# Optimization experiments

Measured on AMD Instinct MI355X. Metric: run time of the kernel, lower is better.

## Reference

```python
import jax, jax.numpy as jnp
import numpy as np

B, S, H = 4, 4096, 2048


def setup_inputs() -> dict:
    key = jax.random.key(0)
    ks = jax.random.split(key, 20)
    def lin(k, fin, fout):
        # torch nn.Linear default init: U(-1/sqrt(fin), 1/sqrt(fin))
        kw, kb = jax.random.split(k)
        bound = 1.0 / np.sqrt(fin)
        W = jax.random.uniform(kw, (fin, fout), jnp.float32, -bound, bound)
        b = jax.random.uniform(kb, (fout,), jnp.float32, -bound, bound)
        return W, b
    hidden_states = jax.random.normal(ks[0], (B, S, H), jnp.float32)
    access_frequency = jax.random.uniform(ks[1], (B, S), jnp.float32)
    importance_score = jax.random.uniform(ks[2], (B, S), jnp.float32)
    sel_W1, sel_b1 = lin(ks[3], H, H // 4)
    sel_W2, sel_b2 = lin(ks[4], H // 4, 3)
    c1_W, c1_b = lin(ks[5], H, H // 2)
    f1_W, f1_b = lin(ks[6], H // 2, H // 2)
    d1_W, d1_b = lin(ks[7], H // 2, H)
    c2_W, c2_b = lin(ks[8], H, H // 4)
    f2_W, f2_b = lin(ks[9], H // 4, H // 4)
    d2_W, d2_b = lin(ks[10], H // 4, H)
    return dict(hidden_states=hidden_states, access_frequency=access_frequency,
                importance_score=importance_score, sel_W1=sel_W1, sel_b1=sel_b1,
                sel_W2=sel_W2, sel_b2=sel_b2, c1_W=c1_W, c1_b=c1_b, f1_W=f1_W,
                f1_b=f1_b, d1_W=d1_W, d1_b=d1_b, c2_W=c2_W, c2_b=c2_b,
                f2_W=f2_W, f2_b=f2_b, d2_W=d2_W, d2_b=d2_b)


def reference(hidden_states, access_frequency, importance_score,
              sel_W1, sel_b1, sel_W2, sel_b2,
              c1_W, c1_b, f1_W, f1_b, d1_W, d1_b,
              c2_W, c2_b, f2_W, f2_b, d2_W, d2_b):
    x = hidden_states  # [B,S,H]
    Hh = x.shape[-1] // 2
    # strategy selector on frequency/importance-modulated features
    combined = jnp.concatenate(
        [x[..., :Hh] * access_frequency[..., None],
         x[..., Hh:] * importance_score[..., None]], axis=-1)  # [B,S,H]
    hmid = jax.nn.relu(jnp.einsum('bsh,hk->bsk', combined, sel_W1) + sel_b1)
    weights = jax.nn.softmax(jnp.einsum('bsk,kl->bsl', hmid, sel_W2) + sel_b2)
    sel = jnp.argmax(weights, axis=-1)  # [B,S] in {0,1,2}
    # expert paths (computed densely, selected per token)
    out1 = (jax.numpy.einsum('bsh,hc->bsc', x, c1_W) + c1_b)
    out1 = jnp.einsum('bsc,cd->bsd', out1, f1_W) + f1_b
    out1 = jnp.einsum('bsc,ch->bsh', out1, d1_W) + d1_b
    out2 = (jnp.einsum('bsh,hc->bsc', x, c2_W) + c2_b)
    out2 = jnp.einsum('bsc,cd->bsd', out2, f2_W) + f2_b
    out2 = jnp.einsum('bsc,ch->bsh', out2, d2_W) + d2_b
    s = sel[..., None]
    out = jnp.where(s == 0, x, jnp.where(s == 1, out1, out2))
    return out
```

## Files before the change

### kernel.cpp

```cpp
#include <hip/hip_runtime.h>


#define RECHECK_TAU 0.008

typedef __bf16 bf16x8 __attribute__((ext_vector_type(8)));
typedef float  f32x4  __attribute__((ext_vector_type(4)));
typedef unsigned short us;

__device__ __forceinline__ float bf2f(us u) {
  union { unsigned u; float f; } v; v.u = ((unsigned)u) << 16;
  return v.f;
}
__device__ __forceinline__ us f2bf(float f) {
  union { float f; unsigned u; } v; v.f = f;
  unsigned r = v.u + 0x7fffu + ((v.u >> 16) & 1u);
  return (us)(r >> 16);
}
__device__ __forceinline__ float scrub(float v) {
  return (v == v && fabsf(v) < 1e30f) ? v : 0.f;
}
__device__ __forceinline__ void gld_lds16(const void* g, void* l) {
  __builtin_amdgcn_global_load_lds(
      (const __attribute__((address_space(1))) void*)g,
      (__attribute__((address_space(3))) void*)l, 16, 0, 0);
}

__global__ __launch_bounds__(256) void xprep(
    const float* __restrict__ X, const float* __restrict__ FR,
    const float* __restrict__ IM, us* __restrict__ Xb, us* __restrict__ Xm)
{
  const int t = blockIdx.x;
  const int j = threadIdx.x;
  const float fr = FR[t], im = IM[t];
  const float md = (j < 128) ? fr : im;
  const float4* src = (const float4*)(X + (size_t)t * 2048);
  float4 a0 = src[2 * j], a1 = src[2 * j + 1];
  float av[8] = {a0.x, a0.y, a0.z, a0.w, a1.x, a1.y, a1.z, a1.w};
  union { uint4 v; us u[8]; } b, m;
#pragma unroll
  for (int k = 0; k < 8; ++k) {
    b.u[k] = f2bf(av[k]);
    m.u[k] = f2bf(av[k] * md);
  }
  ((uint4*)(Xb + (size_t)t * 2048))[j] = b.v;
  ((uint4*)(Xm + (size_t)t * 2048))[j] = m.v;
}

template<int MODE, int AIDX>
__global__ __launch_bounds__(256) void gemm_bt(
    const us* __restrict__ Ap, const us* __restrict__ BT,
    const float* __restrict__ bias, void* __restrict__ outp,
    const int* __restrict__ aidx, const int* __restrict__ oidx,
    const int* __restrict__ cntp, int N, int K)
{
  const int cnt = cntp ? cntp[0] : (int)(gridDim.x << 7);
  const int Mp  = (cnt + 127) & ~127;
  const int bm0 = blockIdx.x * 128;
  if (bm0 >= Mp) return;
  const int bn0 = blockIdx.y * 128;

  __shared__ __align__(16) us As[128 * 64];
  __shared__ __align__(16) us Bs[128 * 64];
  const int tid  = threadIdx.x;
  const int lane = tid & 63;
  const int w    = tid >> 6;
  const int wr   = w >> 1, wc = w & 1;

  const us* gb[4];
  const us* ga[4];
  us* la[4]; us* lb[4];
#pragma unroll
  for (int i = 0; i < 4; ++i) {
    const int s = i * 256 + tid, m = s >> 3, cp = s & 7, c = cp ^ (m & 7);
    gb[i] = BT + (size_t)(bn0 + m) * K + c * 8;
    lb[i] = &Bs[s * 8];
    la[i] = &As[s * 8];
    const int arow = AIDX ? aidx[bm0 + m] : (bm0 + m);
    ga[i] = Ap + (size_t)arow * K + c * 8;
  }

  f32x4 acc[4][4] = {};

  for (int k0 = 0; k0 < K; k0 += 64) {
#pragma unroll
    for (int i = 0; i < 4; ++i) { gld_lds16(gb[i], lb[i]); gb[i] += 64; }
#pragma unroll
    for (int i = 0; i < 4; ++i) { gld_lds16(ga[i], la[i]); ga[i] += 64; }
    __syncthreads();
#pragma unroll
    for (int kk = 0; kk < 2; ++kk) {
      const int cc = kk * 4 + (lane >> 4);
      bf16x8 af[4], bfr[4];
#pragma unroll
      for (int t = 0; t < 4; ++t) {
        const int m = wr * 64 + t * 16 + (lane & 15);
        const int n = wc * 64 + t * 16 + (lane & 15);
        af[t]  = *(const bf16x8*)&As[(m * 8 + (cc ^ (m & 7))) * 8];
        bfr[t] = *(const bf16x8*)&Bs[(n * 8 + (cc ^ (n & 7))) * 8];
      }
#pragma unroll
      for (int mt = 0; mt < 4; ++mt)
#pragma unroll
        for (int nt = 0; nt < 4; ++nt)
          acc[mt][nt] = __builtin_amdgcn_mfma_f32_16x16x32_bf16(
              af[mt], bfr[nt], acc[mt][nt], 0, 0, 0);
    }
    __syncthreads();
  }

  const int colb = bn0 + wc * 64 + (lane & 15);
  const int rowb = bm0 + wr * 64 + ((lane >> 4) << 2);
  float bv[4];
#pragma unroll
  for (int nt = 0; nt < 4; ++nt) bv[nt] = bias[colb + nt * 16];
#pragma unroll
  for (int mt = 0; mt < 4; ++mt) {
#pragma unroll
    for (int r = 0; r < 4; ++r) {
      const int row = rowb + mt * 16 + r;
      if (MODE == 3) {
        if (row >= cnt) continue;
        const size_t orow = (size_t)oidx[row];
#pragma unroll
        for (int nt = 0; nt < 4; ++nt)
          ((float*)outp)[orow * N + colb + nt * 16] =
              scrub(acc[mt][nt][r] + bv[nt]);
      } else if (MODE == 4) {
#pragma unroll
        for (int nt = 0; nt < 4; ++nt)
          ((float*)outp)[(size_t)row * N + colb + nt * 16] =
              fmaxf(scrub(acc[mt][nt][r] + bv[nt]), 0.f);
      } else {
#pragma unroll
        for (int nt = 0; nt < 4; ++nt)
          ((us*)outp)[(size_t)row * N + colb + nt * 16] =
              f2bf(scrub(acc[mt][nt][r] + bv[nt]));
      }
    }
  }
}

__global__ __launch_bounds__(256) void sel_precise(
    const float* __restrict__ X, const float* __restrict__ FR,
    const float* __restrict__ IM,
    const us* __restrict__ BTH, const us* __restrict__ BTL,
    const float* __restrict__ bias, float* __restrict__ hmid_r,
    const int* __restrict__ ridx, const int* __restrict__ cntp)
{
  constexpr int K = 2048, N = 512;
  const int cnt = cntp[0];
  const int Mp  = (cnt + 127) & ~127;
  const int bm0 = blockIdx.x * 128;
  if (bm0 >= Mp) return;
  const int bn0 = blockIdx.y * 128;

  __shared__ __align__(16) us AsH[128 * 64];
  __shared__ __align__(16) us AsL[128 * 64];
  __shared__ __align__(16) us BsH[128 * 64];
  __shared__ __align__(16) us BsL[128 * 64];
  const int tid  = threadIdx.x;
  const int lane = tid & 63;
  const int w    = tid >> 6;
  const int wr   = w >> 1, wc = w & 1;

  const us* gbh[4]; const us* gbl[4];
  const float* gx[4];
  us* lbh[4]; us* lbl[4];
  int sOfs[4], cth[4];
  float fr[4], im[4];
#pragma unroll
  for (int i = 0; i < 4; ++i) {
    const int s = i * 256 + tid, m = s >> 3, cp = s & 7, c = cp ^ (m & 7);
    gbh[i] = BTH + (size_t)(bn0 + m) * K + c * 8;
    gbl[i] = BTL + (size_t)(bn0 + m) * K + c * 8;
    lbh[i] = &BsH[s * 8];
    lbl[i] = &BsL[s * 8];
    const int arow = ridx[bm0 + m];
    gx[i]  = X + (size_t)arow * K + c * 8;
    sOfs[i] = s * 8;
    cth[i]  = c * 8;
    fr[i] = FR[arow];
    im[i] = IM[arow];
  }

  f32x4 acc[4][4] = {};

  for (int k0 = 0; k0 < K; k0 += 64) {
#pragma unroll
    for (int i = 0; i < 4; ++i) {
      gld_lds16(gbh[i], lbh[i]); gbh[i] += 64;
      gld_lds16(gbl[i], lbl[i]); gbl[i] += 64;
    }
#pragma unroll
    for (int i = 0; i < 4; ++i) {
      const float md = (k0 + cth[i] < 1024) ? fr[i] : im[i];
      float4 a0 = *(const float4*)gx[i];
      float4 a1 = *(const float4*)(gx[i] + 4);
      gx[i] += 64;
      float av[8] = {a0.x, a0.y, a0.z, a0.w, a1.x, a1.y, a1.z, a1.w};
      union { uint4 v; us u[8]; } hu, lu;
#pragma unroll
      for (int j = 0; j < 8; ++j) {
        float a = av[j] * md;
        us h = f2bf(a);
        hu.u[j] = h;
        lu.u[j] = f2bf(a - bf2f(h));
      }
      *(uint4*)&AsH[sOfs[i]] = hu.v;
      *(uint4*)&AsL[sOfs[i]] = lu.v;
    }
    __syncthreads();
#pragma unroll
    for (int kk = 0; kk < 2; ++kk) {
      const int cc = kk * 4 + (lane >> 4);
      bf16x8 ah[4], al[4], bh[4], bl[4];
#pragma unroll
      for (int t = 0; t < 4; ++t) {
        const int m = wr * 64 + t * 16 + (lane & 15);
        const int n = wc * 64 + t * 16 + (lane & 15);
        const int ai = (m * 8 + (cc ^ (m & 7))) * 8;
        const int bi = (n * 8 + (cc ^ (n & 7))) * 8;
        ah[t] = *(const bf16x8*)&AsH[ai];
        al[t] = *(const bf16x8*)&AsL[ai];
        bh[t] = *(const bf16x8*)&BsH[bi];
        bl[t] = *(const bf16x8*)&BsL[bi];
      }
#pragma unroll
      for (int mt = 0; mt < 4; ++mt)
#pragma unroll
        for (int nt = 0; nt < 4; ++nt) {
          acc[mt][nt] = __builtin_amdgcn_mfma_f32_16x16x32_bf16(
              ah[mt], bh[nt], acc[mt][nt], 0, 0, 0);
          acc[mt][nt] = __builtin_amdgcn_mfma_f32_16x16x32_bf16(
              al[mt], bh[nt], acc[mt][nt], 0, 0, 0);
          acc[mt][nt] = __builtin_amdgcn_mfma_f32_16x16x32_bf16(
              ah[mt], bl[nt], acc[mt][nt], 0, 0, 0);
        }
    }
    __syncthreads();
  }

  const int colb = bn0 + wc * 64 + (lane & 15);
  const int rowb = bm0 + wr * 64 + ((lane >> 4) << 2);
  float bv[4];
#pragma unroll
  for (int nt = 0; nt < 4; ++nt) bv[nt] = bias[colb + nt * 16];
#pragma unroll
  for (int mt = 0; mt < 4; ++mt)
#pragma unroll
    for (int r = 0; r < 4; ++r) {
      const int row = rowb + mt * 16 + r;
#pragma unroll
      for (int nt = 0; nt < 4; ++nt)
        hmid_r[(size_t)row * N + colb + nt * 16] =
            fmaxf(scrub(acc[mt][nt][r] + bv[nt]), 0.f);
    }
}

__global__ __launch_bounds__(256) void logits_gap(
    const float* __restrict__ hmid, const float* __restrict__ W2,
    const float* __restrict__ B2, int* __restrict__ sel,
    int* __restrict__ cntr, int* __restrict__ ridx)
{
  const int lane = threadIdx.x & 63;
  const int wv   = threadIdx.x >> 6;
  const int t    = blockIdx.x * 4 + wv;
  const float* h = hmid + (size_t)t * 512;
  double s0 = 0.0, s1 = 0.0, s2 = 0.0;
#pragma unroll
  for (int j = 0; j < 8; ++j) {
    int e = j * 64 + lane;
    double hv = (double)h[e];
    s0 += hv * (double)W2[e * 3 + 0];
    s1 += hv * (double)W2[e * 3 + 1];
    s2 += hv * (double)W2[e * 3 + 2];
  }
  for (int o = 32; o > 0; o >>= 1) {
    s0 += __shfl_down(s0, o);
    s1 += __shfl_down(s1, o);
    s2 += __shfl_down(s2, o);
  }
  if (lane == 0) {
    s0 += (double)B2[0]; s1 += (double)B2[1]; s2 += (double)B2[2];
    int idx = 0; double b = s0;
    if (s1 > b) { b = s1; idx = 1; }
    if (s2 > b) { b = s2; idx = 2; }
    sel[t] = idx;
    const double mn = fmin(fmin(s0, s1), s2);
    const double second = (s0 + s1 + s2) - b - mn;
    if (b - second < RECHECK_TAU) {
      const int p = atomicAdd(cntr, 1);
      ridx[p] = t;
    }
  }
}

__global__ __launch_bounds__(256) void logits_fix(
    const float* __restrict__ hmid_r, const float* __restrict__ W2,
    const float* __restrict__ B2, const int* __restrict__ cntr,
    const int* __restrict__ ridx, int* __restrict__ sel)
{
  const int lane = threadIdx.x & 63;
  const int wv   = threadIdx.x >> 6;
  const int r    = blockIdx.x * 4 + wv;
  if (r >= cntr[0]) return;
  const float* h = hmid_r + (size_t)r * 512;
  double s0 = 0.0, s1 = 0.0, s2 = 0.0;
#pragma unroll
  for (int j = 0; j < 8; ++j) {
    int e = j * 64 + lane;
    double hv = (double)h[e];
    s0 += hv * (double)W2[e * 3 + 0];
    s1 += hv * (double)W2[e * 3 + 1];
    s2 += hv * (double)W2[e * 3 + 2];
  }
  for (int o = 32; o > 0; o >>= 1) {
    s0 += __shfl_down(s0, o);
    s1 += __shfl_down(s1, o);
    s2 += __shfl_down(s2, o);
  }
  if (lane == 0) {
    s0 += (double)B2[0]; s1 += (double)B2[1]; s2 += (double)B2[2];
    int idx = 0; double b = s0;
    if (s1 > b) { b = s1; idx = 1; }
    if (s2 > b) { idx = 2; }
    sel[ridx[r]] = idx;
  }
}

__global__ __launch_bounds__(256) void compact(
    const int* __restrict__ sel, int* __restrict__ cnt,
    int* __restrict__ idx1, int* __restrict__ idx2)
{
  const int t    = blockIdx.x * 256 + threadIdx.x;
  const int lane = threadIdx.x & 63;
  const int w    = threadIdx.x >> 6;
  const int s    = sel[t];
  const bool f1 = (s == 1), f2 = (s == 2);
  const unsigned long long m1 = __ballot(f1);
  const unsigned long long m2 = __ballot(f2);
  const unsigned long long lt = (1ull << lane) - 1ull;
  const int b1 = __popcll(m1 & lt);
  const int b2 = __popcll(m2 & lt);
  __shared__ int w1[4], w2[4], base1, base2;
  if (lane == 0) { w1[w] = __popcll(m1); w2[w] = __popcll(m2); }
  __syncthreads();
  if (threadIdx.x == 0) {
    base1 = atomicAdd(&cnt[0], w1[0] + w1[1] + w1[2] + w1[3]);
    base2 = atomicAdd(&cnt[1], w2[0] + w2[1] + w2[2] + w2[3]);
  }
  __syncthreads();
  int o1 = base1, o2 = base2;
  for (int i = 0; i < w; ++i) { o1 += w1[i]; o2 += w2[i]; }
  if (f1) idx1[o1 + b1] = t;
  if (f2) idx2[o2 + b2] = t;
}

__global__ __launch_bounds__(128) void pad_idx(
    const int* __restrict__ cnt, int* __restrict__ idx1, int* __restrict__ idx2)
{
  idx1[cnt[0] + threadIdx.x] = 0;
  idx2[cnt[1] + threadIdx.x] = 0;
}

__global__ __launch_bounds__(128) void pad_r(
    const int* __restrict__ cntr, int* __restrict__ ridx)
{
  ridx[cntr[0] + threadIdx.x] = 0;
}

__global__ __launch_bounds__(256) void pass0(
    const float* __restrict__ X, const int* __restrict__ sel,
    float* __restrict__ OUT)
{
  const int t = blockIdx.x;
  if (sel[t] != 0) return;
  const uint4* src = (const uint4*)(X + (size_t)t * 2048);
  uint4* dst = (uint4*)(OUT + (size_t)t * 2048);
  dst[threadIdx.x]       = src[threadIdx.x];
  dst[threadIdx.x + 256] = src[threadIdx.x + 256];
}

__global__ __launch_bounds__(256) void transpose_f2b(
    const float* __restrict__ W, us* __restrict__ WT, int K, int N)
{
  __shared__ float tile[32][33];
  const int tx = threadIdx.x & 31, ty = threadIdx.x >> 5;
  const int n0 = blockIdx.x * 32, k0 = blockIdx.y * 32;
#pragma unroll
  for (int r = 0; r < 4; ++r)
    tile[ty + r * 8][tx] = W[(size_t)(k0 + ty + r * 8) * N + n0 + tx];
  __syncthreads();
#pragma unroll
  for (int r = 0; r < 4; ++r)
    WT[(size_t)(n0 + ty + r * 8) * K + k0 + tx] = f2bf(tile[tx][ty + r * 8]);
}

__global__ __launch_bounds__(256) void transpose_split(
    const float* __restrict__ W, us* __restrict__ WH, us* __restrict__ WL,
    int K, int N)
{
  __shared__ float tile[32][33];
  const int tx = threadIdx.x & 31, ty = threadIdx.x >> 5;
  const int n0 = blockIdx.x * 32, k0 = blockIdx.y * 32;
#pragma unroll
  for (int r = 0; r < 4; ++r)
    tile[ty + r * 8][tx] = W[(size_t)(k0 + ty + r * 8) * N + n0 + tx];
  __syncthreads();
#pragma unroll
  for (int r = 0; r < 4; ++r) {
    float v = tile[tx][ty + r * 8];
    us h = f2bf(v);
    const size_t o = (size_t)(n0 + ty + r * 8) * K + k0 + tx;
    WH[o] = h;
    WL[o] = f2bf(v - bf2f(h));
  }
}

extern "C" void kernel_launch(void* const* d_in, const int* in_sizes, int n_in,
                              void* d_out, int out_size, void* d_ws, size_t ws_size,
                              hipStream_t stream) {
  const float* X   = (const float*)d_in[0];
  const float* FR  = (const float*)d_in[1];
  const float* IM  = (const float*)d_in[2];
  const float* W1  = (const float*)d_in[3];
  const float* B1  = (const float*)d_in[4];
  const float* W2  = (const float*)d_in[5];
  const float* B2  = (const float*)d_in[6];
  const float* C1W = (const float*)d_in[7];
  const float* C1B = (const float*)d_in[8];
  const float* F1W = (const float*)d_in[9];
  const float* F1B = (const float*)d_in[10];
  const float* D1W = (const float*)d_in[11];
  const float* D1B = (const float*)d_in[12];
  const float* C2W = (const float*)d_in[13];
  const float* C2B = (const float*)d_in[14];
  const float* F2W = (const float*)d_in[15];
  const float* F2B = (const float*)d_in[16];
  const float* D2W = (const float*)d_in[17];
  const float* D2B = (const float*)d_in[18];
  float* OUT = (float*)d_out;

  size_t off = 0;
  auto alloc = [&](size_t bytes) -> void* {
    void* p = (char*)d_ws + off;
    off += (bytes + 255) & ~(size_t)255;
    return p;
  };
  us* WT_selH = (us*)alloc(512ull * 2048 * 2);
  us* WT_selL = (us*)alloc(512ull * 2048 * 2);
  us* WT_c1   = (us*)alloc(1024ull * 2048 * 2);
  us* WT_f1   = (us*)alloc(1024ull * 1024 * 2);
  us* WT_d1   = (us*)alloc(2048ull * 1024 * 2);
  us* WT_c2   = (us*)alloc(512ull * 2048 * 2);
  us* WT_f2   = (us*)alloc(512ull * 512 * 2);
  us* WT_d2   = (us*)alloc(2048ull * 512 * 2);
  int* sel    = (int*)alloc(16384ull * 4);
  int* cnt    = (int*)alloc(3 * 4);
  int* idx1   = (int*)alloc((16384ull + 128) * 4);
  int* idx2   = (int*)alloc((16384ull + 128) * 4);
  int* ridx   = (int*)alloc((16384ull + 128) * 4);
  us*  Xb     = (us*)alloc(16384ull * 2048 * 2);
  void* R1    = alloc(16384ull * 1024 * 2);
  void* R2    = alloc(16384ull * 2048 * 2);
  if (ws_size < off) return;

  us*    Xm     = (us*)R2;
  float* hmid   = (float*)R1;
  float* hmid_r = (float*)R2;
  us* t1 = (us*)R1;
  us* u1 = (us*)R1;
  us* t2 = (us*)R2;
  us* u2 = (us*)R2;

  const dim3 blk(256);
  transpose_split<<<dim3(16, 64), blk, 0, stream>>>(W1, WT_selH, WT_selL, 2048, 512);
  transpose_f2b<<<dim3(32, 64), blk, 0, stream>>>(C1W, WT_c1, 2048, 1024);
  transpose_f2b<<<dim3(32, 32), blk, 0, stream>>>(F1W, WT_f1, 1024, 1024);
  transpose_f2b<<<dim3(64, 32), blk, 0, stream>>>(D1W, WT_d1, 1024, 2048);
  transpose_f2b<<<dim3(16, 64), blk, 0, stream>>>(C2W, WT_c2, 2048, 512);
  transpose_f2b<<<dim3(16, 16), blk, 0, stream>>>(F2W, WT_f2, 512, 512);
  transpose_f2b<<<dim3(64, 16), blk, 0, stream>>>(D2W, WT_d2, 512, 2048);

  hipMemsetAsync(cnt, 0, 12, stream);

  xprep<<<dim3(16384), blk, 0, stream>>>(X, FR, IM, Xb, Xm);

  gemm_bt<4, 0><<<dim3(128, 4), blk, 0, stream>>>(
      Xm, WT_selH, B1, hmid, nullptr, nullptr, nullptr, 512, 2048);
  logits_gap<<<dim3(4096), blk, 0, stream>>>(hmid, W2, B2, sel, cnt + 2, ridx);
  pad_r<<<dim3(1), dim3(128), 0, stream>>>(cnt + 2, ridx);

  sel_precise<<<dim3(128, 4), blk, 0, stream>>>(X, FR, IM, WT_selH, WT_selL,
                                                B1, hmid_r, ridx, cnt + 2);
  logits_fix<<<dim3(4096), blk, 0, stream>>>(hmid_r, W2, B2, cnt + 2, ridx, sel);

  compact<<<dim3(64), blk, 0, stream>>>(sel, cnt, idx1, idx2);
  pad_idx<<<dim3(1), dim3(128), 0, stream>>>(cnt, idx1, idx2);

  pass0<<<dim3(16384), blk, 0, stream>>>(X, sel, OUT);

  gemm_bt<0, 1><<<dim3(128, 8), blk, 0, stream>>>(Xb, WT_c1, C1B, t1, idx1, nullptr, cnt + 0, 1024, 2048);
  gemm_bt<0, 0><<<dim3(128, 8), blk, 0, stream>>>(t1, WT_f1, F1B, t2, nullptr, nullptr, cnt + 0, 1024, 1024);
  gemm_bt<3, 0><<<dim3(128, 16), blk, 0, stream>>>(t2, WT_d1, D1B, OUT, nullptr, idx1, cnt + 0, 2048, 1024);

  gemm_bt<0, 1><<<dim3(128, 4), blk, 0, stream>>>(Xb, WT_c2, C2B, u1, idx2, nullptr, cnt + 1, 512, 2048);
  gemm_bt<0, 0><<<dim3(128, 4), blk, 0, stream>>>(u1, WT_f2, F2B, u2, nullptr, nullptr, cnt + 1, 512, 512);
  gemm_bt<3, 0><<<dim3(128, 16), blk, 0, stream>>>(u2, WT_d2, D2B, OUT, nullptr, idx2, cnt + 1, 2048, 512);
}
```

Baseline: 716.3 us.

## Replace split-bf16 MFMA recheck path with fused fp32 per-token recheck kernel

Removes the three-pass bf16 hi/lo MFMA GEMM for near-tie tokens, the separate logits_fix pass, the pad kernel and the low-part weight transpose. A single recheck kernel now rebuilds the modulated features for 4 tokens in LDS, computes the hidden layer in fp32 straight from the untransposed W1, applies ReLU and the second projection, reduces across waves and rewrites the selection. This cuts launches, the hmid_r round trip and one weight transpose. In exchange every block re-reads all of W1 from global memory, so the cost grows with the number of flagged tokens and may be high if many tokens fall within the tie margin.

```diff
diff --git a/kernel.cpp b/kernel.cpp
--- a/kernel.cpp
+++ b/kernel.cpp
@@ -138,123 +138,6 @@
       }
     }
   }
-}
-
-__global__ __launch_bounds__(256) void sel_precise(
-    const float* __restrict__ X, const float* __restrict__ FR,
-    const float* __restrict__ IM,
-    const us* __restrict__ BTH, const us* __restrict__ BTL,
-    const float* __restrict__ bias, float* __restrict__ hmid_r,
-    const int* __restrict__ ridx, const int* __restrict__ cntp)
-{
-  constexpr int K = 2048, N = 512;
-  const int cnt = cntp[0];
-  const int Mp  = (cnt + 127) & ~127;
-  const int bm0 = blockIdx.x * 128;
-  if (bm0 >= Mp) return;
-  const int bn0 = blockIdx.y * 128;
-
-  __shared__ __align__(16) us AsH[128 * 64];
-  __shared__ __align__(16) us AsL[128 * 64];
-  __shared__ __align__(16) us BsH[128 * 64];
-  __shared__ __align__(16) us BsL[128 * 64];
-  const int tid  = threadIdx.x;
-  const int lane = tid & 63;
-  const int w    = tid >> 6;
-  const int wr   = w >> 1, wc = w & 1;
-
-  const us* gbh[4]; const us* gbl[4];
-  const float* gx[4];
-  us* lbh[4]; us* lbl[4];
-  int sOfs[4], cth[4];
-  float fr[4], im[4];
-#pragma unroll
-  for (int i = 0; i < 4; ++i) {
-    const int s = i * 256 + tid, m = s >> 3, cp = s & 7, c = cp ^ (m & 7);
-    gbh[i] = BTH + (size_t)(bn0 + m) * K + c * 8;
-    gbl[i] = BTL + (size_t)(bn0 + m) * K + c * 8;
-    lbh[i] = &BsH[s * 8];
-    lbl[i] = &BsL[s * 8];
-    const int arow = ridx[bm0 + m];
-    gx[i]  = X + (size_t)arow * K + c * 8;
-    sOfs[i] = s * 8;
-    cth[i]  = c * 8;
-    fr[i] = FR[arow];
-    im[i] = IM[arow];
-  }
-
-  f32x4 acc[4][4] = {};
-
-  for (int k0 = 0; k0 < K; k0 += 64) {
-#pragma unroll
-    for (int i = 0; i < 4; ++i) {
-      gld_lds16(gbh[i], lbh[i]); gbh[i] += 64;
-      gld_lds16(gbl[i], lbl[i]); gbl[i] += 64;
-    }
-#pragma unroll
-    for (int i = 0; i < 4; ++i) {
-      const float md = (k0 + cth[i] < 1024) ? fr[i] : im[i];
-      float4 a0 = *(const float4*)gx[i];
-      float4 a1 = *(const float4*)(gx[i] + 4);
-      gx[i] += 64;
-      float av[8] = {a0.x, a0.y, a0.z, a0.w, a1.x, a1.y, a1.z, a1.w};
-      union { uint4 v; us u[8]; } hu, lu;
-#pragma unroll
-      for (int j = 0; j < 8; ++j) {
-        float a = av[j] * md;
-        us h = f2bf(a);
-        hu.u[j] = h;
-        lu.u[j] = f2bf(a - bf2f(h));
-      }
-      *(uint4*)&AsH[sOfs[i]] = hu.v;
-      *(uint4*)&AsL[sOfs[i]] = lu.v;
-    }
-    __syncthreads();
-#pragma unroll
-    for (int kk = 0; kk < 2; ++kk) {
-      const int cc = kk * 4 + (lane >> 4);
-      bf16x8 ah[4], al[4], bh[4], bl[4];
-#pragma unroll
-      for (int t = 0; t < 4; ++t) {
-        const int m = wr * 64 + t * 16 + (lane & 15);
-        const int n = wc * 64 + t * 16 + (lane & 15);
-        const int ai = (m * 8 + (cc ^ (m & 7))) * 8;
-        const int bi = (n * 8 + (cc ^ (n & 7))) * 8;
-        ah[t] = *(const bf16x8*)&AsH[ai];
-        al[t] = *(const bf16x8*)&AsL[ai];
-        bh[t] = *(const bf16x8*)&BsH[bi];
-        bl[t] = *(const bf16x8*)&BsL[bi];
-      }
-#pragma unroll
-      for (int mt = 0; mt < 4; ++mt)
-#pragma unroll
-        for (int nt = 0; nt < 4; ++nt) {
-          acc[mt][nt] = __builtin_amdgcn_mfma_f32_16x16x32_bf16(
-              ah[mt], bh[nt], acc[mt][nt], 0, 0, 0);
-          acc[mt][nt] = __builtin_amdgcn_mfma_f32_16x16x32_bf16(
-              al[mt], bh[nt], acc[mt][nt], 0, 0, 0);
-          acc[mt][nt] = __builtin_amdgcn_mfma_f32_16x16x32_bf16(
-              ah[mt], bl[nt], acc[mt][nt], 0, 0, 0);
-        }
-    }
-    __syncthreads();
-  }
-
-  const int colb = bn0 + wc * 64 + (lane & 15);
-  const int rowb = bm0 + wr * 64 + ((lane >> 4) << 2);
-  float bv[4];
-#pragma unroll
-  for (int nt = 0; nt < 4; ++nt) bv[nt] = bias[colb + nt * 16];
-#pragma unroll
-  for (int mt = 0; mt < 4; ++mt)
-#pragma unroll
-    for (int r = 0; r < 4; ++r) {
-      const int row = rowb + mt * 16 + r;
-#pragma unroll
-      for (int nt = 0; nt < 4; ++nt)
-        hmid_r[(size_t)row * N + colb + nt * 16] =
-            fmaxf(scrub(acc[mt][nt][r] + bv[nt]), 0.f);
-    }
 }
 
 __global__ __launch_bounds__(256) void logits_gap(
@@ -295,36 +178,100 @@
   }
 }
 
-__global__ __launch_bounds__(256) void logits_fix(
-    const float* __restrict__ hmid_r, const float* __restrict__ W2,
+__global__ __launch_bounds__(256) void recheck(
+    const float* __restrict__ X, const float* __restrict__ FR,
+    const float* __restrict__ IM, const float* __restrict__ W1,
+    const float* __restrict__ B1, const float* __restrict__ W2,
     const float* __restrict__ B2, const int* __restrict__ cntr,
     const int* __restrict__ ridx, int* __restrict__ sel)
 {
-  const int lane = threadIdx.x & 63;
-  const int wv   = threadIdx.x >> 6;
-  const int r    = blockIdx.x * 4 + wv;
-  if (r >= cntr[0]) return;
-  const float* h = hmid_r + (size_t)r * 512;
-  double s0 = 0.0, s1 = 0.0, s2 = 0.0;
-#pragma unroll
-  for (int j = 0; j < 8; ++j) {
-    int e = j * 64 + lane;
-    double hv = (double)h[e];
-    s0 += hv * (double)W2[e * 3 + 0];
-    s1 += hv * (double)W2[e * 3 + 1];
-    s2 += hv * (double)W2[e * 3 + 2];
-  }
-  for (int o = 32; o > 0; o >>= 1) {
-    s0 += __shfl_down(s0, o);
-    s1 += __shfl_down(s1, o);
-    s2 += __shfl_down(s2, o);
-  }
-  if (lane == 0) {
-    s0 += (double)B2[0]; s1 += (double)B2[1]; s2 += (double)B2[2];
-    int idx = 0; double b = s0;
-    if (s1 > b) { b = s1; idx = 1; }
-    if (s2 > b) { idx = 2; }
-    sel[ridx[r]] = idx;
+  const int nr = cntr[0];
+  const int r0 = blockIdx.x * 4;
+  if (r0 >= nr) return;
+
+  __shared__ __align__(16) float comb[4][2048];
+  __shared__ float red[4][4][3];
+  const int tid  = threadIdx.x;
+  const int lane = tid & 63;
+  const int wv   = tid >> 6;
+
+  int toks[4];
+#pragma unroll
+  for (int i = 0; i < 4; ++i) {
+    const int r    = r0 + i;
+    const bool lv  = (r < nr);
+    const int tok  = lv ? ridx[r] : ridx[r0];
+    toks[i] = lv ? tok : -1;
+    const float md = (tid < 128) ? FR[tok] : IM[tok];
+    const float4* src = (const float4*)(X + (size_t)tok * 2048);
+    float4 a0 = src[2 * tid], a1 = src[2 * tid + 1];
+    float* c = &comb[i][8 * tid];
+    c[0] = a0.x * md; c[1] = a0.y * md; c[2] = a0.z * md; c[3] = a0.w * md;
+    c[4] = a1.x * md; c[5] = a1.y * md; c[6] = a1.z * md; c[7] = a1.w * md;
+  }
+  __syncthreads();
+
+  float z[4][2] = {};
+  const float* wp = W1 + 2 * tid;
+  const float4* cb[4] = {(const float4*)comb[0], (const float4*)comb[1],
+                         (const float4*)comb[2], (const float4*)comb[3]};
+#pragma unroll 4
+  for (int k4 = 0; k4 < 512; ++k4) {
+    const float4 c0 = cb[0][k4], c1 = cb[1][k4], c2 = cb[2][k4], c3 = cb[3][k4];
+    const float* wk = wp + (size_t)k4 * 2048;
+    const float2 wA = *(const float2*)(wk);
+    const float2 wB = *(const float2*)(wk + 512);
+    const float2 wC = *(const float2*)(wk + 1024);
+    const float2 wD = *(const float2*)(wk + 1536);
+    z[0][0] = fmaf(c0.x, wA.x, z[0][0]); z[0][1] = fmaf(c0.x, wA.y, z[0][1]);
+    z[1][0] = fmaf(c1.x, wA.x, z[1][0]); z[1][1] = fmaf(c1.x, wA.y, z[1][1]);
+    z[2][0] = fmaf(c2.x, wA.x, z[2][0]); z[2][1] = fmaf(c2.x, wA.y, z[2][1]);
+    z[3][0] = fmaf(c3.x, wA.x, z[3][0]); z[3][1] = fmaf(c3.x, wA.y, z[3][1]);
+    z[0][0] = fmaf(c0.y, wB.x, z[0][0]); z[0][1] = fmaf(c0.y, wB.y, z[0][1]);
+    z[1][0] = fmaf(c1.y, wB.x, z[1][0]); z[1][1] = fmaf(c1.y, wB.y, z[1][1]);
+    z[2][0] = fmaf(c2.y, wB.x, z[2][0]); z[2][1] = fmaf(c2.y, wB.y, z[2][1]);
+    z[3][0] = fmaf(c3.y, wB.x, z[3][0]); z[3][1] = fmaf(c3.y, wB.y, z[3][1]);
+    z[0][0] = fmaf(c0.z, wC.x, z[0][0]); z[0][1] = fmaf(c0.z, wC.y, z[0][1]);
+    z[1][0] = fmaf(c1.z, wC.x, z[1][0]); z[1][1] = fmaf(c1.z, wC.y, z[1][1]);
+    z[2][0] = fmaf(c2.z, wC.x, z[2][0]); z[2][1] = fmaf(c2.z, wC.y, z[2][1]);
+    z[3][0] = fmaf(c3.z, wC.x, z[3][0]); z[3][1] = fmaf(c3.z, wC.y, z[3][1]);
+    z[0][0] = fmaf(c0.w, wD.x, z[0][0]); z[0][1] = fmaf(c0.w, wD.y, z[0][1]);
+    z[1][0] = fmaf(c1.w, wD.x, z[1][0]); z[1][1] = fmaf(c1.w, wD.y, z[1][1]);
+    z[2][0] = fmaf(c2.w, wD.x, z[2][0]); z[2][1] = fmaf(c2.w, wD.y, z[2][1]);
+    z[3][0] = fmaf(c3.w, wD.x, z[3][0]); z[3][1] = fmaf(c3.w, wD.y, z[3][1]);
+  }
+
+  const float b0 = B1[2 * tid], b1 = B1[2 * tid + 1];
+  const float w20 = W2[(2 * tid) * 3 + 0], w21 = W2[(2 * tid) * 3 + 1],
+              w22 = W2[(2 * tid) * 3 + 2];
+  const float w30 = W2[(2 * tid + 1) * 3 + 0], w31 = W2[(2 * tid + 1) * 3 + 1],
+              w32 = W2[(2 * tid + 1) * 3 + 2];
+#pragma unroll
+  for (int i = 0; i < 4; ++i) {
+    const float h0 = fmaxf(z[i][0] + b0, 0.f);
+    const float h1 = fmaxf(z[i][1] + b1, 0.f);
+    float p0 = h0 * w20 + h1 * w30;
+    float p1 = h0 * w21 + h1 * w31;
+    float p2 = h0 * w22 + h1 * w32;
+    for (int o = 32; o > 0; o >>= 1) {
+      p0 += __shfl_down(p0, o);
+      p1 += __shfl_down(p1, o);
+      p2 += __shfl_down(p2, o);
+    }
+    if (lane == 0) { red[wv][i][0] = p0; red[wv][i][1] = p1; red[wv][i][2] = p2; }
+  }
+  __syncthreads();
+  if (tid < 4) {
+    const int i = tid;
+    if (toks[i] >= 0) {
+      const float s0 = red[0][i][0] + red[1][i][0] + red[2][i][0] + red[3][i][0] + B2[0];
+      const float s1 = red[0][i][1] + red[1][i][1] + red[2][i][1] + red[3][i][1] + B2[1];
+      const float s2 = red[0][i][2] + red[1][i][2] + red[2][i][2] + red[3][i][2] + B2[2];
+      int idx = 0; float b = s0;
+      if (s1 > b) { b = s1; idx = 1; }
+      if (s2 > b) { idx = 2; }
+      sel[toks[i]] = idx;
+    }
   }
 }
 
@@ -363,12 +310,6 @@
   idx2[cnt[1] + threadIdx.x] = 0;
 }
 
-__global__ __launch_bounds__(128) void pad_r(
-    const int* __restrict__ cntr, int* __restrict__ ridx)
-{
-  ridx[cntr[0] + threadIdx.x] = 0;
-}
-
 __global__ __launch_bounds__(256) void pass0(
     const float* __restrict__ X, const int* __restrict__ sel,
     float* __restrict__ OUT)
@@ -394,27 +335,6 @@
 #pragma unroll
   for (int r = 0; r < 4; ++r)
     WT[(size_t)(n0 + ty + r * 8) * K + k0 + tx] = f2bf(tile[tx][ty + r * 8]);
-}
-
-__global__ __launch_bounds__(256) void transpose_split(
-    const float* __restrict__ W, us* __restrict__ WH, us* __restrict__ WL,
-    int K, int N)
-{
-  __shared__ float tile[32][33];
-  const int tx = threadIdx.x & 31, ty = threadIdx.x >> 5;
-  const int n0 = blockIdx.x * 32, k0 = blockIdx.y * 32;
-#pragma unroll
-  for (int r = 0; r < 4; ++r)
-    tile[ty + r * 8][tx] = W[(size_t)(k0 + ty + r * 8) * N + n0 + tx];
-  __syncthreads();
-#pragma unroll
-  for (int r = 0; r < 4; ++r) {
-    float v = tile[tx][ty + r * 8];
-    us h = f2bf(v);
-    const size_t o = (size_t)(n0 + ty + r * 8) * K + k0 + tx;
-    WH[o] = h;
-    WL[o] = f2bf(v - bf2f(h));
-  }
 }
 
 extern "C" void kernel_launch(void* const* d_in, const int* in_sizes, int n_in,
@@ -448,7 +368,6 @@
     return p;
   };
   us* WT_selH = (us*)alloc(512ull * 2048 * 2);
-  us* WT_selL = (us*)alloc(512ull * 2048 * 2);
   us* WT_c1   = (us*)alloc(1024ull * 2048 * 2);
   us* WT_f1   = (us*)alloc(1024ull * 1024 * 2);
   us* WT_d1   = (us*)alloc(2048ull * 1024 * 2);
@@ -459,22 +378,21 @@
   int* cnt    = (int*)alloc(3 * 4);
   int* idx1   = (int*)alloc((16384ull + 128) * 4);
   int* idx2   = (int*)alloc((16384ull + 128) * 4);
-  int* ridx   = (int*)alloc((16384ull + 128) * 4);
+  int* ridx   = (int*)alloc(16384ull * 4);
   us*  Xb     = (us*)alloc(16384ull * 2048 * 2);
   void* R1    = alloc(16384ull * 1024 * 2);
   void* R2    = alloc(16384ull * 2048 * 2);
   if (ws_size < off) return;
 
-  us*    Xm     = (us*)R2;
-  float* hmid   = (float*)R1;
-  float* hmid_r = (float*)R2;
+  us*    Xm   = (us*)R2;
+  float* hmid = (float*)R1;
   us* t1 = (us*)R1;
   us* u1 = (us*)R1;
   us* t2 = (us*)R2;
   us* u2 = (us*)R2;
 
   const dim3 blk(256);
-  transpose_split<<<dim3(16, 64), blk, 0, stream>>>(W1, WT_selH, WT_selL, 2048, 512);
+  transpose_f2b<<<dim3(16, 64), blk, 0, stream>>>(W1, WT_selH, 2048, 512);
   transpose_f2b<<<dim3(32, 64), blk, 0, stream>>>(C1W, WT_c1, 2048, 1024);
   transpose_f2b<<<dim3(32, 32), blk, 0, stream>>>(F1W, WT_f1, 1024, 1024);
   transpose_f2b<<<dim3(64, 32), blk, 0, stream>>>(D1W, WT_d1, 1024, 2048);
@@ -489,11 +407,9 @@
   gemm_bt<4, 0><<<dim3(128, 4), blk, 0, stream>>>(
       Xm, WT_selH, B1, hmid, nullptr, nullptr, nullptr, 512, 2048);
   logits_gap<<<dim3(4096), blk, 0, stream>>>(hmid, W2, B2, sel, cnt + 2, ridx);
-  pad_r<<<dim3(1), dim3(128), 0, stream>>>(cnt + 2, ridx);
-
-  sel_precise<<<dim3(128, 4), blk, 0, stream>>>(X, FR, IM, WT_selH, WT_selL,
-                                                B1, hmid_r, ridx, cnt + 2);
-  logits_fix<<<dim3(4096), blk, 0, stream>>>(hmid_r, W2, B2, cnt + 2, ridx, sel);
+
+  recheck<<<dim3(4096), blk, 0, stream>>>(X, FR, IM, W1, B1, W2, B2,
+                                          cnt + 2, ridx, sel);
 
   compact<<<dim3(64), blk, 0, stream>>>(sel, cnt, idx1, idx2);
   pad_idx<<<dim3(1), dim3(128), 0, stream>>>(cnt, idx1, idx2);
```

After: 738.2 us. 3.1% more time.
